# Optimization experiments

Hardware: AMD Instinct MI355X
Metric: run time of the kernel (lower is better)

## Reference

```python
import jax, jax.numpy as jnp
import numpy as np

N_NODES = 100000
N_EDGES = 3200000
N_FEAT = 256
N_FILT = 256


def setup_inputs() -> dict:
    key = jax.random.key(0)
    k1, k2, k3, k4, k5 = jax.random.split(key, 5)
    # Xavier-normal-ish filters: std = sqrt(2/(fan_in+fan_out))
    std = (2.0 / (N_FEAT + N_FILT)) ** 0.5
    filters = jax.random.normal(k1, (N_FEAT, N_FILT), dtype=jnp.float32) * std
    x = jax.random.normal(k2, (N_NODES, N_FEAT), dtype=jnp.float32)
    edge_row = jax.random.randint(k3, (N_EDGES,), 0, N_NODES, dtype=jnp.int32)
    edge_col = jax.random.randint(k4, (N_EDGES,), 0, N_NODES, dtype=jnp.int32)
    edge_weight = jax.random.uniform(k5, (N_EDGES,), dtype=jnp.float32)
    return {"x": x, "filters": filters, "edge_row": edge_row,
            "edge_col": edge_col, "edge_weight": edge_weight}


def reference(x, filters, edge_row, edge_col, edge_weight):
    # XF = x @ filters  -> [N, K]
    XF = jnp.matmul(x, filters)
    # out = transform @ XF, transform given in COO form:
    # out[r] = sum_{e: row[e]==r} weight[e] * XF[col[e]]
    msgs = edge_weight[:, None] * XF[edge_col]          # [E, K] gather
    out = jax.ops.segment_sum(msgs, edge_row, num_segments=N_NODES)  # [N, K] scatter-add
    return out
```

## Files before the change

kernel.cpp:

```cpp
#include <hip/hip_runtime.h>

#define NF 256
#define NK 256
#define NBKT 512
#define TILEA 8192

typedef __attribute__((ext_vector_type(8))) short bf16x8;
typedef __attribute__((ext_vector_type(4))) float f32x4;

__device__ __forceinline__ ushort f2bf(float f) {
  uint u = __float_as_uint(f);
  return (ushort)((u + 0x7fffu + ((u >> 16) & 1u)) >> 16);
}
__device__ __forceinline__ float bf2f(ushort h) {
  return __uint_as_float(((uint)h) << 16);
}

__global__ __launch_bounds__(256) void prelude(const float* __restrict__ F,
                                               ushort* __restrict__ Ft,
                                               const int* __restrict__ erow,
                                               int* __restrict__ bcnt, int nE) {
  __shared__ int h[NBKT];
  if (blockIdx.x < NF) {
    int k = blockIdx.x;
    int n = threadIdx.x;
    Ft[(size_t)n * NF + k] = f2bf(F[(size_t)k * NK + n]);
    return;
  }
  const int bid = blockIdx.x - NF;
  const int nb = gridDim.x - NF;
  h[threadIdx.x] = 0;
  h[threadIdx.x + 256] = 0;
  __syncthreads();
  for (int e = bid * 256 + threadIdx.x; e < nE; e += nb * 256)
    atomicAdd(&h[erow[e] >> 8], 1);
  __syncthreads();
  int v0 = h[threadIdx.x], v1 = h[threadIdx.x + 256];
  if (v0) atomicAdd(&bcnt[threadIdx.x], v0);
  if (v1) atomicAdd(&bcnt[threadIdx.x + 256], v1);
}

__global__ __launch_bounds__(256) void gemm_mfma(const float* __restrict__ x,
                                                 const ushort* __restrict__ Ft,
                                                 ushort* __restrict__ XFh, int M) {
  __shared__ ushort As[64 * NF];
  const int t = threadIdx.x;
  const int row0 = blockIdx.x * 64;

  const float4* xv = (const float4*)(x + (size_t)row0 * NF);
#pragma unroll
  for (int j = 0; j < 16; ++j) {
    int idx = j * 256 + t;
    int r = idx >> 6;
    int c4 = idx & 63;
    float4 v = make_float4(0.f, 0.f, 0.f, 0.f);
    if (row0 + r < M) v = xv[idx];
    ushort4 hh = make_ushort4(f2bf(v.x), f2bf(v.y), f2bf(v.z), f2bf(v.w));
    uint boff = (uint)(r * 512 + c4 * 8);
    boff ^= (uint)((r & 7) << 4);
    *(ushort4*)((char*)As + boff) = hh;
  }
  __syncthreads();

  const int lane = t & 63;
  const int wv = t >> 6;
  const int arow = lane & 15;
  const int kg = lane >> 4;
  const int ncol0 = wv * 64;

#pragma unroll
  for (int rt = 0; rt < 4; ++rt) {
    bf16x8 afr[8];
#pragma unroll
    for (int kk = 0; kk < 8; ++kk) {
      int r = rt * 16 + arow;
      uint boff = (uint)(r * 512 + kk * 64 + kg * 16);
      boff ^= (uint)((r & 7) << 4);
      afr[kk] = *(const bf16x8*)((const char*)As + boff);
    }

    f32x4 acc[4];
#pragma unroll
    for (int f = 0; f < 4; ++f) acc[f] = (f32x4){0.f, 0.f, 0.f, 0.f};

#pragma unroll
    for (int f = 0; f < 4; ++f) {
      const ushort* bp = Ft + (size_t)(ncol0 + f * 16 + arow) * NF + kg * 8;
#pragma unroll
      for (int kk = 0; kk < 8; ++kk) {
        bf16x8 bfr = *(const bf16x8*)(bp + kk * 32);
        acc[f] = __builtin_amdgcn_mfma_f32_16x16x32_bf16(afr[kk], bfr, acc[f], 0, 0, 0);
      }
    }

#pragma unroll
    for (int f = 0; f < 4; ++f) {
      int col = ncol0 + f * 16 + arow;
#pragma unroll
      for (int rg = 0; rg < 4; ++rg) {
        int row = row0 + rt * 16 + kg * 4 + rg;
        if (row < M) XFh[(size_t)row * NK + col] = f2bf(acc[f][rg]);
      }
    }
  }
}

__global__ __launch_bounds__(512) void scan_bbase(const int* __restrict__ bcnt,
                                                  int* __restrict__ bbase,
                                                  int* __restrict__ bcursor) {
  __shared__ int s[NBKT];
  int t = threadIdx.x;
  int v = bcnt[t];
  s[t] = v;
  __syncthreads();
  for (int d = 1; d < NBKT; d <<= 1) {
    int tmp = (t >= d) ? s[t - d] : 0;
    __syncthreads();
    s[t] += tmp;
    __syncthreads();
  }
  int excl = s[t] - v;
  bbase[t] = excl;
  bcursor[t * 16] = excl;
}

__global__ __launch_bounds__(512) void bin_coarse(const int* __restrict__ erow,
                                                  const int* __restrict__ ecol,
                                                  const float* __restrict__ ew,
                                                  int* __restrict__ bcursor,
                                                  int2* __restrict__ tmpCW, int nE) {
  __shared__ int h[NBKT];
  __shared__ int lb[NBKT];
  __shared__ int gb[NBKT];
  __shared__ int2 pay[TILEA];
  const int t = threadIdx.x;
  const int base = blockIdx.x * TILEA;

  h[t] = 0;
  __syncthreads();

  int rnk[16], bb[16], loc[16];
#pragma unroll
  for (int k = 0; k < 16; ++k) {
    int i = base + k * 512 + t;
    rnk[k] = -1; bb[k] = 0; loc[k] = 0;
    if (i < nE) {
      int row = erow[i];
      bb[k] = row >> 8;
      loc[k] = row & 255;
      rnk[k] = atomicAdd(&h[bb[k]], 1);
    }
  }
  __syncthreads();

  int hv = h[t];
  lb[t] = hv;
  __syncthreads();
  for (int d = 1; d < NBKT; d <<= 1) {
    int tmp = (t >= d) ? lb[t - d] : 0;
    __syncthreads();
    lb[t] += tmp;
    __syncthreads();
  }
  int ex = lb[t] - hv;
  __syncthreads();
  lb[t] = ex;
  if (hv > 0) gb[t] = atomicAdd(&bcursor[t * 16], hv);
  __syncthreads();

#pragma unroll
  for (int k = 0; k < 16; ++k) {
    int i = base + k * 512 + t;
    if (i < nE) {
      int pos = lb[bb[k]] + rnk[k];
      pay[pos] = make_int2(ecol[i] | (loc[k] << 20), __float_as_int(ew[i]));
    }
  }
  __syncthreads();

  const int wv = t >> 6, lane = t & 63;
  for (int b = wv; b < NBKT; b += 8) {
    int len = h[b];
    if (!len) continue;
    int lbase = lb[b], gbase = gb[b];
    for (int off = lane; off < len; off += 64)
      tmpCW[gbase + off] = pay[lbase + off];
  }
}

__global__ __launch_bounds__(256) void bin_fine(const int2* __restrict__ tmpCW,
                                                const int* __restrict__ bbase,
                                                const int* __restrict__ bcnt,
                                                int* __restrict__ offsets,
                                                int2* __restrict__ cw,
                                                int nNodes, int nE) {
  __shared__ int hist[256];
  __shared__ int cur[256];
  const int b = blockIdx.x;
  const int t = threadIdx.x;
  const int base = bbase[b];
  const int n = bcnt[b];

  hist[t] = 0;
  __syncthreads();
  for (int i = t; i < n; i += 256)
    atomicAdd(&hist[((uint)tmpCW[base + i].x) >> 20], 1);
  __syncthreads();

  int hv = hist[t];
  cur[t] = hv;
  __syncthreads();
  for (int d = 1; d < 256; d <<= 1) {
    int tmp = (t >= d) ? cur[t - d] : 0;
    __syncthreads();
    cur[t] += tmp;
    __syncthreads();
  }
  int ex = cur[t] - hv;
  __syncthreads();
  cur[t] = ex;
  int node = (b << 8) + t;
  if (node < nNodes) offsets[node] = base + ex;
  if (b == 0 && t == 0) offsets[nNodes] = nE;
  __syncthreads();

  for (int i = t; i < n; i += 256) {
    int2 v = tmpCW[base + i];
    int local = ((uint)v.x) >> 20;
    int d = base + atomicAdd(&cur[local], 1);
    cw[d] = make_int2(v.x & 0xFFFFF, v.y);
  }
}

__global__ __launch_bounds__(256) void gather_bf16(const ushort* __restrict__ XFh,
                                                   const int* __restrict__ offsets,
                                                   const int2* __restrict__ cw,
                                                   f32x4* __restrict__ outv,
                                                   int nNodes) {
  const int lane = threadIdx.x & 63;
  const int node = (blockIdx.x * blockDim.x + threadIdx.x) >> 6;
  if (node >= nNodes) return;
  const int start = offsets[node];
  const int end = offsets[node + 1];
  const ushort4* XV = (const ushort4*)XFh;

  float ax = 0.f, ay = 0.f, az = 0.f, aw = 0.f;
  for (int base = start; base < end; base += 64) {
    int n = end - base;
    if (n > 64) n = 64;
    int2 e = make_int2(0, 0);
    if (lane < n) {
      long long raw = __builtin_nontemporal_load((const long long*)(cw + base + lane));
      e.x = (int)(raw & 0xFFFFFFFFll);
      e.y = (int)(raw >> 32);
    }
    int skey = (lane < n) ? ((e.x << 6) | lane) : ((0xFFFFF << 6) | lane);
    int sval = e.y;
#pragma unroll
    for (int k = 2; k <= 64; k <<= 1) {
#pragma unroll
      for (int j = k >> 1; j > 0; j >>= 1) {
        int pk = __shfl_xor(skey, j);
        int pv = __shfl_xor(sval, j);
        bool take_min = ((lane & k) == 0) == ((lane & j) == 0);
        bool keep = (take_min == (skey < pk));
        skey = keep ? skey : pk;
        sval = keep ? sval : pv;
      }
    }
    e.x = ((uint)skey) >> 6;
    e.y = sval;

    int j = 0;
    for (; j + 7 < n; j += 8) {
      int c0 = __shfl(e.x, j),     c1 = __shfl(e.x, j + 1);
      int c2 = __shfl(e.x, j + 2), c3 = __shfl(e.x, j + 3);
      int c4 = __shfl(e.x, j + 4), c5 = __shfl(e.x, j + 5);
      int c6 = __shfl(e.x, j + 6), c7 = __shfl(e.x, j + 7);
      float w0 = __int_as_float(__shfl(e.y, j));
      float w1 = __int_as_float(__shfl(e.y, j + 1));
      float w2 = __int_as_float(__shfl(e.y, j + 2));
      float w3 = __int_as_float(__shfl(e.y, j + 3));
      float w4 = __int_as_float(__shfl(e.y, j + 4));
      float w5 = __int_as_float(__shfl(e.y, j + 5));
      float w6 = __int_as_float(__shfl(e.y, j + 6));
      float w7 = __int_as_float(__shfl(e.y, j + 7));
      ushort4 v0 = XV[(size_t)c0 * 64 + lane];
      ushort4 v1 = XV[(size_t)c1 * 64 + lane];
      ushort4 v2 = XV[(size_t)c2 * 64 + lane];
      ushort4 v3 = XV[(size_t)c3 * 64 + lane];
      ushort4 v4 = XV[(size_t)c4 * 64 + lane];
      ushort4 v5 = XV[(size_t)c5 * 64 + lane];
      ushort4 v6 = XV[(size_t)c6 * 64 + lane];
      ushort4 v7 = XV[(size_t)c7 * 64 + lane];
      ax += w0 * bf2f(v0.x); ay += w0 * bf2f(v0.y); az += w0 * bf2f(v0.z); aw += w0 * bf2f(v0.w);
      ax += w1 * bf2f(v1.x); ay += w1 * bf2f(v1.y); az += w1 * bf2f(v1.z); aw += w1 * bf2f(v1.w);
      ax += w2 * bf2f(v2.x); ay += w2 * bf2f(v2.y); az += w2 * bf2f(v2.z); aw += w2 * bf2f(v2.w);
      ax += w3 * bf2f(v3.x); ay += w3 * bf2f(v3.y); az += w3 * bf2f(v3.z); aw += w3 * bf2f(v3.w);
      ax += w4 * bf2f(v4.x); ay += w4 * bf2f(v4.y); az += w4 * bf2f(v4.z); aw += w4 * bf2f(v4.w);
      ax += w5 * bf2f(v5.x); ay += w5 * bf2f(v5.y); az += w5 * bf2f(v5.z); aw += w5 * bf2f(v5.w);
      ax += w6 * bf2f(v6.x); ay += w6 * bf2f(v6.y); az += w6 * bf2f(v6.z); aw += w6 * bf2f(v6.w);
      ax += w7 * bf2f(v7.x); ay += w7 * bf2f(v7.y); az += w7 * bf2f(v7.z); aw += w7 * bf2f(v7.w);
    }
    for (; j + 3 < n; j += 4) {
      int c0 = __shfl(e.x, j),     c1 = __shfl(e.x, j + 1);
      int c2 = __shfl(e.x, j + 2), c3 = __shfl(e.x, j + 3);
      float w0 = __int_as_float(__shfl(e.y, j));
      float w1 = __int_as_float(__shfl(e.y, j + 1));
      float w2 = __int_as_float(__shfl(e.y, j + 2));
      float w3 = __int_as_float(__shfl(e.y, j + 3));
      ushort4 v0 = XV[(size_t)c0 * 64 + lane];
      ushort4 v1 = XV[(size_t)c1 * 64 + lane];
      ushort4 v2 = XV[(size_t)c2 * 64 + lane];
      ushort4 v3 = XV[(size_t)c3 * 64 + lane];
      ax += w0 * bf2f(v0.x); ay += w0 * bf2f(v0.y); az += w0 * bf2f(v0.z); aw += w0 * bf2f(v0.w);
      ax += w1 * bf2f(v1.x); ay += w1 * bf2f(v1.y); az += w1 * bf2f(v1.z); aw += w1 * bf2f(v1.w);
      ax += w2 * bf2f(v2.x); ay += w2 * bf2f(v2.y); az += w2 * bf2f(v2.z); aw += w2 * bf2f(v2.w);
      ax += w3 * bf2f(v3.x); ay += w3 * bf2f(v3.y); az += w3 * bf2f(v3.z); aw += w3 * bf2f(v3.w);
    }
    for (; j < n; ++j) {
      int c0 = __shfl(e.x, j);
      float w0 = __int_as_float(__shfl(e.y, j));
      ushort4 v0 = XV[(size_t)c0 * 64 + lane];
      ax += w0 * bf2f(v0.x); ay += w0 * bf2f(v0.y); az += w0 * bf2f(v0.z); aw += w0 * bf2f(v0.w);
    }
  }
  f32x4 r; r.x = ax; r.y = ay; r.z = az; r.w = aw;
  __builtin_nontemporal_store(r, &outv[(size_t)node * 64 + lane]);
}

__global__ __launch_bounds__(256) void gemm_xf(const float* __restrict__ x,
                                               const float* __restrict__ F,
                                               float* __restrict__ XF, int M) {
  __shared__ float xs[64][NF];
  const int t = threadIdx.x;
  const int row0 = blockIdx.x * 64;
  const int rows = min(64, M - row0);
  const float4* xv = (const float4*)(x + (size_t)row0 * NF);
  float4* xsv = (float4*)&xs[0][0];
#pragma unroll
  for (int j = 0; j < 16; ++j) {
    int i = j * 256 + t;
    int r = i >> 6;
    float4 v;
    if (r < rows) v = xv[i];
    else          v = make_float4(0.f, 0.f, 0.f, 0.f);
    xsv[i] = v;
  }
  __syncthreads();
  const int r0 = (t >> 5) * 8;
  const int c0 = blockIdx.y * 128 + (t & 31) * 4;
  float acc[8][4];
#pragma unroll
  for (int r = 0; r < 8; ++r)
#pragma unroll
    for (int c = 0; c < 4; ++c) acc[r][c] = 0.f;
  for (int k = 0; k < NF; k += 4) {
    float4 f0 = *(const float4*)(F + (size_t)(k + 0) * NK + c0);
    float4 f1 = *(const float4*)(F + (size_t)(k + 1) * NK + c0);
    float4 f2 = *(const float4*)(F + (size_t)(k + 2) * NK + c0);
    float4 f3 = *(const float4*)(F + (size_t)(k + 3) * NK + c0);
#pragma unroll
    for (int r = 0; r < 8; ++r) {
      float4 xr = *(const float4*)&xs[r0 + r][k];
      acc[r][0] += xr.x * f0.x + xr.y * f1.x + xr.z * f2.x + xr.w * f3.x;
      acc[r][1] += xr.x * f0.y + xr.y * f1.y + xr.z * f2.y + xr.w * f3.y;
      acc[r][2] += xr.x * f0.z + xr.y * f1.z + xr.z * f2.z + xr.w * f3.z;
      acc[r][3] += xr.x * f0.w + xr.y * f1.w + xr.z * f2.w + xr.w * f3.w;
    }
  }
#pragma unroll
  for (int r = 0; r < 8; ++r) {
    int row = r0 + r;
    if (row < rows) {
      float4 v = make_float4(acc[r][0], acc[r][1], acc[r][2], acc[r][3]);
      *(float4*)(XF + (size_t)(row0 + row) * NK + c0) = v;
    }
  }
}

__global__ __launch_bounds__(256) void scatter_edges(
    const float* __restrict__ XF, const int* __restrict__ erow,
    const int* __restrict__ ecol, const float* __restrict__ ew,
    float* __restrict__ out, int nE) {
  const int lane = threadIdx.x & 63;
  const int wid = (blockIdx.x * blockDim.x + threadIdx.x) >> 6;
  const int nwaves = (gridDim.x * blockDim.x) >> 6;
  for (int e = wid; e < nE; e += nwaves) {
    const int r = erow[e];
    const int c = ecol[e];
    const float w = ew[e];
    float4 v = *(const float4*)(XF + (size_t)c * NK + lane * 4);
    float* dst = out + (size_t)r * NK + lane * 4;
    atomicAdd(dst + 0, w * v.x);
    atomicAdd(dst + 1, w * v.y);
    atomicAdd(dst + 2, w * v.z);
    atomicAdd(dst + 3, w * v.w);
  }
}

static inline size_t align16(size_t x) { return (x + 15) & ~(size_t)15; }

extern "C" void kernel_launch(void* const* d_in, const int* in_sizes, int n_in,
                              void* d_out, int out_size, void* d_ws, size_t ws_size,
                              hipStream_t stream) {
  const float* x  = (const float*)d_in[0];
  const float* F  = (const float*)d_in[1];
  const int* erow = (const int*)d_in[2];
  const int* ecol = (const int*)d_in[3];
  const float* ew = (const float*)d_in[4];
  float* out      = (float*)d_out;

  const int M      = in_sizes[0] / NF;
  const int nE     = in_sizes[2];
  const int nNodes = out_size / NK;

  char* base = (char*)d_ws;
  size_t off = 0;
  ushort* XFh  = (ushort*)(base + off); off += align16((size_t)M * NK * sizeof(ushort));
  ushort* Ft   = (ushort*)(base + off); off += align16((size_t)NF * NK * sizeof(ushort));
  int* offsets = (int*)(base + off);    off += align16(((size_t)nNodes + 1) * sizeof(int));
  int* bcnt    = (int*)(base + off);    off += align16(NBKT * sizeof(int));
  int* bbase   = (int*)(base + off);    off += align16(NBKT * sizeof(int));
  int* bcursor = (int*)(base + off);    off += align16((size_t)NBKT * 16 * sizeof(int));
  int2* tmpCW  = (int2*)(base + off);   off += align16((size_t)nE * sizeof(int2));
  int2* cw     = (int2*)(base + off);   off += align16((size_t)nE * sizeof(int2));
  const size_t needed = off;

  const int nb2 = (nNodes + 255) >> 8;
  const bool ok = (ws_size >= needed) && (nb2 <= NBKT) &&
                  (nNodes < (1 << 20)) && (M < (1 << 20));

  if (ok) {
    hipMemsetAsync(bcnt, 0, NBKT * sizeof(int), stream);
    prelude<<<NF + 2048, 256, 0, stream>>>(F, Ft, erow, bcnt, nE);
    gemm_mfma<<<(M + 63) / 64, 256, 0, stream>>>(x, Ft, XFh, M);
    scan_bbase<<<1, NBKT, 0, stream>>>(bcnt, bbase, bcursor);
    bin_coarse<<<(nE + TILEA - 1) / TILEA, 512, 0, stream>>>(erow, ecol, ew,
                                                             bcursor, tmpCW, nE);
    bin_fine<<<nb2, 256, 0, stream>>>(tmpCW, bbase, bcnt, offsets, cw, nNodes, nE);
    int gblocks = (nNodes + 3) / 4;
    gather_bf16<<<gblocks, 256, 0, stream>>>(XFh, offsets, cw, (f32x4*)out, nNodes);
  } else {
    float* XF = (float*)d_ws;
    dim3 gg((M + 63) / 64, NK / 128);
    gemm_xf<<<gg, 256, 0, stream>>>(x, F, XF, M);
    hipMemsetAsync(d_out, 0, (size_t)out_size * sizeof(float), stream);
    scatter_edges<<<2048, 256, 0, stream>>>(XF, erow, ecol, ew, out, nE);
  }
}
```

Before: 417.5 us.

## Fuse GEMM and coarse edge binning into one heterogeneous launch

```diff
diff --git a/kernel.cpp b/kernel.cpp
--- a/kernel.cpp
+++ b/kernel.cpp
@@ -40,17 +40,101 @@
   if (v1) atomicAdd(&bcnt[threadIdx.x + 256], v1);
 }
 
-__global__ __launch_bounds__(256) void gemm_mfma(const float* __restrict__ x,
-                                                 const ushort* __restrict__ Ft,
-                                                 ushort* __restrict__ XFh, int M) {
-  __shared__ ushort As[64 * NF];
+__global__ __launch_bounds__(512) void scan_bbase(const int* __restrict__ bcnt,
+                                                  int* __restrict__ bbase,
+                                                  int* __restrict__ bcursor) {
+  __shared__ int s[NBKT];
+  int t = threadIdx.x;
+  int v = bcnt[t];
+  s[t] = v;
+  __syncthreads();
+  for (int d = 1; d < NBKT; d <<= 1) {
+    int tmp = (t >= d) ? s[t - d] : 0;
+    __syncthreads();
+    s[t] += tmp;
+    __syncthreads();
+  }
+  int excl = s[t] - v;
+  bbase[t] = excl;
+  bcursor[t * 16] = excl;
+}
+
+__global__ __launch_bounds__(512) void fused_gemm_bin(
+    const float* __restrict__ x, const ushort* __restrict__ Ft,
+    ushort* __restrict__ XFh, int M,
+    const int* __restrict__ erow, const int* __restrict__ ecol,
+    const float* __restrict__ ew, int* __restrict__ bcursor,
+    int2* __restrict__ tmpCW, int nE, int nBin) {
+  __shared__ __align__(16) char lds[6 * 1024 + TILEA * 8];
   const int t = threadIdx.x;
-  const int row0 = blockIdx.x * 64;
+
+  if ((int)blockIdx.x < nBin) {
+    int* h  = (int*)lds;
+    int* lb = h + NBKT;
+    int* gb = lb + NBKT;
+    int2* pay = (int2*)(gb + NBKT);
+    const int base = blockIdx.x * TILEA;
+
+    h[t] = 0;
+    __syncthreads();
+
+    int rnk[16], bb[16], loc[16];
+#pragma unroll
+    for (int k = 0; k < 16; ++k) {
+      int i = base + k * 512 + t;
+      rnk[k] = -1; bb[k] = 0; loc[k] = 0;
+      if (i < nE) {
+        int row = erow[i];
+        bb[k] = row >> 8;
+        loc[k] = row & 255;
+        rnk[k] = atomicAdd(&h[bb[k]], 1);
+      }
+    }
+    __syncthreads();
+
+    int hv = h[t];
+    lb[t] = hv;
+    __syncthreads();
+    for (int d = 1; d < NBKT; d <<= 1) {
+      int tmp = (t >= d) ? lb[t - d] : 0;
+      __syncthreads();
+      lb[t] += tmp;
+      __syncthreads();
+    }
+    int ex = lb[t] - hv;
+    __syncthreads();
+    lb[t] = ex;
+    if (hv > 0) gb[t] = atomicAdd(&bcursor[t * 16], hv);
+    __syncthreads();
+
+#pragma unroll
+    for (int k = 0; k < 16; ++k) {
+      int i = base + k * 512 + t;
+      if (i < nE) {
+        int pos = lb[bb[k]] + rnk[k];
+        pay[pos] = make_int2(ecol[i] | (loc[k] << 20), __float_as_int(ew[i]));
+      }
+    }
+    __syncthreads();
+
+    const int wv = t >> 6, lane = t & 63;
+    for (int b = wv; b < NBKT; b += 8) {
+      int len = h[b];
+      if (!len) continue;
+      int lbase = lb[b], gbase = gb[b];
+      for (int off = lane; off < len; off += 64)
+        tmpCW[gbase + off] = pay[lbase + off];
+    }
+    return;
+  }
+
+  ushort* As = (ushort*)lds;
+  const int row0 = ((int)blockIdx.x - nBin) * 128;
 
   const float4* xv = (const float4*)(x + (size_t)row0 * NF);
 #pragma unroll
   for (int j = 0; j < 16; ++j) {
-    int idx = j * 256 + t;
+    int idx = j * 512 + t;
     int r = idx >> 6;
     int c4 = idx & 63;
     float4 v = make_float4(0.f, 0.f, 0.f, 0.f);
@@ -58,25 +142,28 @@
     ushort4 hh = make_ushort4(f2bf(v.x), f2bf(v.y), f2bf(v.z), f2bf(v.w));
     uint boff = (uint)(r * 512 + c4 * 8);
     boff ^= (uint)((r & 7) << 4);
-    *(ushort4*)((char*)As + boff) = hh;
+    *(ushort4*)(lds + boff) = hh;
   }
   __syncthreads();
 
   const int lane = t & 63;
   const int wv = t >> 6;
+  const int half = wv >> 2;
+  const int wq = wv & 3;
   const int arow = lane & 15;
   const int kg = lane >> 4;
-  const int ncol0 = wv * 64;
+  const int ncol0 = wq * 64;
 
 #pragma unroll
   for (int rt = 0; rt < 4; ++rt) {
+    const int rbase = half * 64 + rt * 16;
     bf16x8 afr[8];
 #pragma unroll
     for (int kk = 0; kk < 8; ++kk) {
-      int r = rt * 16 + arow;
+      int r = rbase + arow;
       uint boff = (uint)(r * 512 + kk * 64 + kg * 16);
       boff ^= (uint)((r & 7) << 4);
-      afr[kk] = *(const bf16x8*)((const char*)As + boff);
+      afr[kk] = *(const bf16x8*)(lds + boff);
     }
 
     f32x4 acc[4];
@@ -98,93 +185,10 @@
       int col = ncol0 + f * 16 + arow;
 #pragma unroll
       for (int rg = 0; rg < 4; ++rg) {
-        int row = row0 + rt * 16 + kg * 4 + rg;
+        int row = row0 + rbase + kg * 4 + rg;
         if (row < M) XFh[(size_t)row * NK + col] = f2bf(acc[f][rg]);
       }
     }
-  }
-}
-
-__global__ __launch_bounds__(512) void scan_bbase(const int* __restrict__ bcnt,
-                                                  int* __restrict__ bbase,
-                                                  int* __restrict__ bcursor) {
-  __shared__ int s[NBKT];
-  int t = threadIdx.x;
-  int v = bcnt[t];
-  s[t] = v;
-  __syncthreads();
-  for (int d = 1; d < NBKT; d <<= 1) {
-    int tmp = (t >= d) ? s[t - d] : 0;
-    __syncthreads();
-    s[t] += tmp;
-    __syncthreads();
-  }
-  int excl = s[t] - v;
-  bbase[t] = excl;
-  bcursor[t * 16] = excl;
-}
-
-__global__ __launch_bounds__(512) void bin_coarse(const int* __restrict__ erow,
-                                                  const int* __restrict__ ecol,
-                                                  const float* __restrict__ ew,
-                                                  int* __restrict__ bcursor,
-                                                  int2* __restrict__ tmpCW, int nE) {
-  __shared__ int h[NBKT];
-  __shared__ int lb[NBKT];
-  __shared__ int gb[NBKT];
-  __shared__ int2 pay[TILEA];
-  const int t = threadIdx.x;
-  const int base = blockIdx.x * TILEA;
-
-  h[t] = 0;
-  __syncthreads();
-
-  int rnk[16], bb[16], loc[16];
-#pragma unroll
-  for (int k = 0; k < 16; ++k) {
-    int i = base + k * 512 + t;
-    rnk[k] = -1; bb[k] = 0; loc[k] = 0;
-    if (i < nE) {
-      int row = erow[i];
-      bb[k] = row >> 8;
-      loc[k] = row & 255;
-      rnk[k] = atomicAdd(&h[bb[k]], 1);
-    }
-  }
-  __syncthreads();
-
-  int hv = h[t];
-  lb[t] = hv;
-  __syncthreads();
-  for (int d = 1; d < NBKT; d <<= 1) {
-    int tmp = (t >= d) ? lb[t - d] : 0;
-    __syncthreads();
-    lb[t] += tmp;
-    __syncthreads();
-  }
-  int ex = lb[t] - hv;
-  __syncthreads();
-  lb[t] = ex;
-  if (hv > 0) gb[t] = atomicAdd(&bcursor[t * 16], hv);
-  __syncthreads();
-
-#pragma unroll
-  for (int k = 0; k < 16; ++k) {
-    int i = base + k * 512 + t;
-    if (i < nE) {
-      int pos = lb[bb[k]] + rnk[k];
-      pay[pos] = make_int2(ecol[i] | (loc[k] << 20), __float_as_int(ew[i]));
-    }
-  }
-  __syncthreads();
-
-  const int wv = t >> 6, lane = t & 63;
-  for (int b = wv; b < NBKT; b += 8) {
-    int len = h[b];
-    if (!len) continue;
-    int lbase = lb[b], gbase = gb[b];
-    for (int off = lane; off < len; off += 64)
-      tmpCW[gbase + off] = pay[lbase + off];
   }
 }
 
@@ -434,10 +438,11 @@
   if (ok) {
     hipMemsetAsync(bcnt, 0, NBKT * sizeof(int), stream);
     prelude<<<NF + 2048, 256, 0, stream>>>(F, Ft, erow, bcnt, nE);
-    gemm_mfma<<<(M + 63) / 64, 256, 0, stream>>>(x, Ft, XFh, M);
     scan_bbase<<<1, NBKT, 0, stream>>>(bcnt, bbase, bcursor);
-    bin_coarse<<<(nE + TILEA - 1) / TILEA, 512, 0, stream>>>(erow, ecol, ew,
-                                                             bcursor, tmpCW, nE);
+    const int nBin = (nE + TILEA - 1) / TILEA;
+    const int nGemm = (M + 127) / 128;
+    fused_gemm_bin<<<nBin + nGemm, 512, 0, stream>>>(x, Ft, XFh, M, erow, ecol,
+                                                     ew, bcursor, tmpCW, nE, nBin);
     bin_fine<<<nb2, 256, 0, stream>>>(tmpCW, bbase, bcnt, offsets, cw, nNodes, nE);
     int gblocks = (nNodes + 3) / 4;
     gather_bf16<<<gblocks, 256, 0, stream>>>(XFh, offsets, cw, (f32x4*)out, nNodes);
```

Result: no change. 417.6 us (+0.0%).
